# Optimization experiments

Hardware: AMD Instinct MI355X
Metric: run time of the kernel (lower is better)

Reference implementation:

```python
import jax, jax.numpy as jnp
import numpy as np

D_MODEL = 512
N_HEADS = 8
D_HEAD = D_MODEL // N_HEADS
SCALE = D_HEAD ** -0.5


def _rel_shift(x):
    # x: (b, h, qlen, klen) -> Transformer-XL relative shift
    b, h, qlen, klen = x.shape
    x = jnp.pad(x, ((0, 0), (0, 0), (0, 0), (1, 0)))        # (b,h,q,k+1)
    x = x.reshape(b, h, klen + 1, qlen)
    x = x[:, :, 1:, :].reshape(b, h, qlen, klen)
    return x


def setup_inputs() -> dict:
    key = jax.random.key(0)
    ks = jax.random.split(key, 12)
    B, S = 2, 2048
    P = 2 * S - 1
    w = lambda k, shape: (jax.random.normal(k, shape, jnp.float32) * 0.02)
    return {
        "x": jax.random.normal(ks[0], (B, S, D_MODEL), jnp.float32),
        "pos_emb": jax.random.normal(ks[1], (P, D_MODEL), jnp.float32),
        "Wq": w(ks[2], (D_MODEL, D_MODEL)), "bq": jnp.zeros((D_MODEL,), jnp.float32),
        "Wk": w(ks[3], (D_MODEL, D_MODEL)), "bk": jnp.zeros((D_MODEL,), jnp.float32),
        "Wv": w(ks[4], (D_MODEL, D_MODEL)), "bv": jnp.zeros((D_MODEL,), jnp.float32),
        "Wp": w(ks[5], (D_MODEL, D_MODEL)),
        "Wo": w(ks[6], (D_MODEL, D_MODEL)), "bo": jnp.zeros((D_MODEL,), jnp.float32),
        "pos_bias_u": w(ks[7], (N_HEADS, D_HEAD)),
        "pos_bias_v": w(ks[8], (N_HEADS, D_HEAD)),
    }


def reference(x, pos_emb, Wq, bq, Wk, bk, Wv, bv, Wp, Wo, bo, pos_bias_u, pos_bias_v):
    B, S, _ = x.shape
    # projections (torch Linear: y = x @ W^T + b; here W stored as (in, out))
    q = (x @ Wq + bq).reshape(B, S, N_HEADS, D_HEAD)
    k = (x @ Wk + bk).reshape(B, S, N_HEADS, D_HEAD)
    v = (x @ Wv + bv).reshape(B, S, N_HEADS, D_HEAD)
    p = (pos_emb @ Wp).reshape(-1, N_HEADS, D_HEAD)  # (2S-1, H, D)

    # content score: (q + u) @ k^T  -> (B,H,S,S)
    content = jnp.einsum("bshd,bthd->bhst", q + pos_bias_u, k)
    # position score: (q + v_bias) @ p^T -> (B,H,S,2S-1), then rel_shift
    pos = jnp.einsum("bshd,phd->bhsp", q + pos_bias_v, p)
    pos = _rel_shift(pos)[..., :S]  # trim to kv_len

    attn = jax.nn.softmax((content + pos) * SCALE, axis=-1)
    out = jnp.einsum("bhst,bthd->bshd", attn, v).reshape(B, S, D_MODEL)
    out = out @ Wo + bo
    return out
```

## Files before the change

### kernel.cpp

```cpp
#include <hip/hip_runtime.h>

#define DM    512
#define NH    8
#define DH    64
#define SEQ   2048
#define PLEN  4095
#define NB    2
#define ATT_SCALE 0.125f

typedef __attribute__((ext_vector_type(8))) _Float16 half8;
typedef __attribute__((ext_vector_type(4))) float   floatx4;

__device__ __forceinline__ void gll16(const _Float16* g, _Float16* l) {
    __builtin_amdgcn_global_load_lds(
        (const __attribute__((address_space(1))) void*)g,
        (__attribute__((address_space(3))) void*)l, 16, 0, 0);
}

__global__ __launch_bounds__(256)
void prep(const float* __restrict__ x, const float* __restrict__ pe,
          const float* __restrict__ W0, const float* __restrict__ W1,
          const float* __restrict__ W2, const float* __restrict__ W3,
          const float* __restrict__ W4,
          _Float16* __restrict__ x16, _Float16* __restrict__ pe16,
          _Float16* __restrict__ Wt)
{
    __shared__ _Float16 tile[64 * 72];
    const int z = blockIdx.z;
    const int t = threadIdx.x;

    if (z < 2) {
        const float* src = z ? pe : x;
        _Float16* dst = z ? pe16 : x16;
        const long n = z ? (long)PLEN * DM : (long)NB * SEQ * DM;
        const long i = ((long)blockIdx.x * 256 + t) * 8;
        if (i >= n) return;
        float4 f0 = *(const float4*)(src + i);
        float4 f1 = *(const float4*)(src + i + 4);
        half8 o;
        o[0] = (_Float16)f0.x; o[1] = (_Float16)f0.y;
        o[2] = (_Float16)f0.z; o[3] = (_Float16)f0.w;
        o[4] = (_Float16)f1.x; o[5] = (_Float16)f1.y;
        o[6] = (_Float16)f1.z; o[7] = (_Float16)f1.w;
        *(half8*)(dst + i) = o;
        return;
    }
    if (blockIdx.x >= 64) return;
    const int wz = z - 2;
    const float* W = (wz == 0) ? W0 : (wz == 1) ? W1 : (wz == 2) ? W2
                   : (wz == 3) ? W3 : W4;
    _Float16* dst_base = Wt + (size_t)wz * DM * DM;
    const int n0 = (blockIdx.x & 7) * 64, k0 = (blockIdx.x >> 3) * 64;
    {
        const int kr = t >> 2, nch = (t & 3) * 16;
        const float* src = W + (size_t)(k0 + kr) * DM + n0 + nch;
        float4 f0 = *(const float4*)(src + 0);
        float4 f1 = *(const float4*)(src + 4);
        float4 f2 = *(const float4*)(src + 8);
        float4 f3 = *(const float4*)(src + 12);
        _Float16* trow = &tile[kr * 72 + nch];
        trow[0]  = (_Float16)f0.x; trow[1]  = (_Float16)f0.y;
        trow[2]  = (_Float16)f0.z; trow[3]  = (_Float16)f0.w;
        trow[4]  = (_Float16)f1.x; trow[5]  = (_Float16)f1.y;
        trow[6]  = (_Float16)f1.z; trow[7]  = (_Float16)f1.w;
        trow[8]  = (_Float16)f2.x; trow[9]  = (_Float16)f2.y;
        trow[10] = (_Float16)f2.z; trow[11] = (_Float16)f2.w;
        trow[12] = (_Float16)f3.x; trow[13] = (_Float16)f3.y;
        trow[14] = (_Float16)f3.z; trow[15] = (_Float16)f3.w;
    }
    __syncthreads();
    {
        const int nr = t >> 2, kch = (t & 3) * 16;
        half8 o0, o1;
#pragma unroll
        for (int i = 0; i < 8; ++i) o0[i] = tile[(kch + i) * 72 + nr];
#pragma unroll
        for (int i = 0; i < 8; ++i) o1[i] = tile[(kch + 8 + i) * 72 + nr];
        _Float16* dst = dst_base + (size_t)(n0 + nr) * DM + k0 + kch;
        *(half8*)dst = o0;
        *(half8*)(dst + 8) = o1;
    }
}

__global__ __launch_bounds__(256)
void gemm_qkvp(const _Float16* __restrict__ X, const _Float16* __restrict__ Pe,
               const _Float16* __restrict__ Wt,
               const float* __restrict__ bq, const float* __restrict__ bk,
               const float* __restrict__ bv, const float* __restrict__ bu,
               const float* __restrict__ bvb,
               _Float16* __restrict__ qu16, _Float16* __restrict__ qv16,
               _Float16* __restrict__ k16, _Float16* __restrict__ vt16,
               _Float16* __restrict__ p16)
{
    __shared__ _Float16 smem[32768];

    const int t = threadIdx.x;
    const int w = t >> 6, lane = t & 63, quad = lane >> 4, l16 = lane & 15;
    const int wr = w >> 1, wc = w & 1;
    const int l3 = lane >> 3, pos = lane & 7;
    const int z = blockIdx.z;
    const int n0 = blockIdx.x * 128;
    const int m0 = blockIdx.y * 128;

    const _Float16* A = (z == 3) ? Pe : X;
    const _Float16* Wz = Wt + (size_t)z * DM * DM;

    const int kx = l16 & 7;
    const int hox0 = ((quad) ^ kx) * 8;
    const int hox1 = ((4 + quad) ^ kx) * 8;

    floatx4 acc[4][4];
#pragma unroll
    for (int i = 0; i < 4; ++i)
#pragma unroll
        for (int j = 0; j < 4; ++j) acc[i][j] = (floatx4){0.f, 0.f, 0.f, 0.f};

#define QSTAGE(CUR, K0)                                                        \
    { _Float16* aB = smem + (CUR) * 16384;                                     \
      _Float16* wB = aB + 8192;                                                \
      _Pragma("unroll") for (int I = 0; I < 4; ++I) {                          \
        const int gr = I * 32 + w * 8 + l3;                                    \
        const int ch = pos ^ l3;                                               \
        int ar = m0 + gr; if (z == 3 && ar > PLEN - 1) ar = PLEN - 1;          \
        gll16(A + (size_t)ar * DM + (K0) + ch * 8, aB + I * 2048 + w * 512);   \
        gll16(Wz + (size_t)(n0 + gr) * DM + (K0) + ch * 8,                     \
              wB + I * 2048 + w * 512); } }

    QSTAGE(0, 0);
    int cur = 0;
    for (int k0 = 0; k0 < DM; k0 += 64) {
        asm volatile("s_waitcnt vmcnt(0)" ::: "memory");
        __builtin_amdgcn_s_barrier();
        asm volatile("" ::: "memory");
        if (k0 + 64 < DM) QSTAGE(cur ^ 1, k0 + 64);
        const _Float16* aB = smem + cur * 16384;
        const _Float16* wB = aB + 8192;
#pragma unroll
        for (int kb = 0; kb < 2; ++kb) {
            const int hox = kb ? hox1 : hox0;
            half8 af[4], bf[4];
#pragma unroll
            for (int i = 0; i < 4; ++i)
                af[i] = *(const half8*)&aB[(wr * 64 + i * 16 + l16) * 64 + hox];
#pragma unroll
            for (int j = 0; j < 4; ++j)
                bf[j] = *(const half8*)&wB[(wc * 64 + j * 16 + l16) * 64 + hox];
#pragma unroll
            for (int i = 0; i < 4; ++i)
#pragma unroll
                for (int j = 0; j < 4; ++j)
                    acc[i][j] = __builtin_amdgcn_mfma_f32_16x16x32_f16(
                        af[i], bf[j], acc[i][j], 0, 0, 0);
        }
        cur ^= 1;
    }
#undef QSTAGE

    const int hh = (n0 >> 6) + wc;
    const int bb = m0 >> 11;
    const int sbase = (m0 & 2047) + wr * 64;

    if (z == 0) {
#pragma unroll
        for (int j = 0; j < 4; ++j) {
            const int n = n0 + wc * 64 + j * 16 + l16;
            const float bval = bq[n], uval = bu[n], vval = bvb[n];
#pragma unroll
            for (int i = 0; i < 4; ++i)
#pragma unroll
                for (int r = 0; r < 4; ++r) {
                    const int s = sbase + i * 16 + 4 * quad + r;
                    const size_t dst = ((size_t)((hh * NB + bb) * SEQ) + s) * DH + (n & 63);
                    const float q = acc[i][j][r] + bval;
                    qu16[dst] = (_Float16)((q + uval) * ATT_SCALE);
                    qv16[dst] = (_Float16)((q + vval) * ATT_SCALE);
                }
        }
    } else if (z == 1) {
#pragma unroll
        for (int j = 0; j < 4; ++j) {
            const int n = n0 + wc * 64 + j * 16 + l16;
            const float bval = bk[n];
#pragma unroll
            for (int i = 0; i < 4; ++i)
#pragma unroll
                for (int r = 0; r < 4; ++r) {
                    const int s = sbase + i * 16 + 4 * quad + r;
                    k16[((size_t)((hh * NB + bb) * SEQ) + s) * DH + (n & 63)] =
                        (_Float16)(acc[i][j][r] + bval);
                }
        }
    } else if (z == 2) {
        __syncthreads();
        _Float16* tr = smem;
#pragma unroll
        for (int j = 0; j < 4; ++j) {
            const int ncol = wc * 64 + j * 16 + l16;
            const float bval = bv[n0 + ncol];
#pragma unroll
            for (int i = 0; i < 4; ++i)
#pragma unroll
                for (int r = 0; r < 4; ++r)
                    tr[(wr * 64 + i * 16 + 4 * quad + r) * 132 + ncol] =
                        (_Float16)(acc[i][j][r] + bval);
        }
        __syncthreads();
        {
            const int col = t >> 1;
            const int half = t & 1;
            const int h2 = (n0 + col) >> 6, d = (n0 + col) & 63;
            const int s0 = (m0 & 2047) + half * 64;
            _Float16* dst = vt16 + ((size_t)((h2 * NB + bb) * DH) + d) * SEQ + s0;
#pragma unroll
            for (int c = 0; c < 8; ++c) {
                half8 o;
#pragma unroll
                for (int k = 0; k < 8; ++k)
                    o[k] = tr[(half * 64 + c * 8 + k) * 132 + col];
                *(half8*)(dst + c * 8) = o;
            }
        }
    } else {
#pragma unroll
        for (int j = 0; j < 4; ++j) {
            const int n = n0 + wc * 64 + j * 16 + l16;
#pragma unroll
            for (int i = 0; i < 4; ++i)
#pragma unroll
                for (int r = 0; r < 4; ++r) {
                    const int m = m0 + wr * 64 + i * 16 + 4 * quad + r;
                    if (m < PLEN)
                        p16[((size_t)hh * PLEN + m) * DH + (n & 63)] =
                            (_Float16)acc[i][j][r];
                }
        }
    }
}

__global__ __launch_bounds__(256, 3)
void relattn_mfma(const _Float16* __restrict__ QU,
                  const _Float16* __restrict__ QV,
                  const _Float16* __restrict__ Kp,
                  const _Float16* __restrict__ VT,
                  const _Float16* __restrict__ Pp,
                  float* __restrict__ Opart,
                  float* __restrict__ Lpart)
{
    __shared__ _Float16 kbuf[2 * 4096];
    __shared__ _Float16 vbuf[4096];
    __shared__ _Float16 pring[2 * 4096];
    __shared__ _Float16 tS[64 * 72];

    const int t = threadIdx.x;
    const int w = t >> 6, lane = t & 63, quad = lane >> 4, l16 = lane & 15;

    const int bid = blockIdx.x;
    const int swz = (bid & 7) * 128 + (bid >> 3);
    const int i0 = (swz & 31) * 64;
    const int h  = (swz >> 5) & 7;
    const int zz = swz >> 8;
    const int b = zz & 1, jh = zz >> 1;

    const size_t hb = (size_t)(h * NB + b);
    const int cbase = 48 - 16 * w;
    const int jbeg = jh * (SEQ / 2), jend = jbeg + (SEQ / 2);

    half8 qa[2], va[2];
    {
        const _Float16* qrow = QU + (hb * SEQ + i0 + 16 * w + l16) * DH + quad * 8;
        const _Float16* vrow = QV + (hb * SEQ + i0 + 16 * w + l16) * DH + quad * 8;
        qa[0] = *(const half8*)qrow;       qa[1] = *(const half8*)(qrow + 32);
        va[0] = *(const half8*)vrow;       va[1] = *(const half8*)(vrow + 32);
    }

    floatx4 O[4];
    float lsum[4] = {0.f, 0.f, 0.f, 0.f};
#pragma unroll
    for (int ct = 0; ct < 4; ++ct) O[ct] = (floatx4){0.f, 0.f, 0.f, 0.f};

    const _Float16* Kbase = Kp + hb * SEQ * DH;
    const _Float16* Vbase = VT + hb * DH * SEQ;
    const _Float16* Pbase = Pp + (size_t)h * PLEN * DH;
    const int rbase0 = (SEQ - 1) - i0 - 63;
    const int w0beg  = rbase0 + jbeg;

    const int kx = l16 & 7;
    const int hox0 = ((quad) ^ kx) * 8;
    const int hox1 = ((4 + quad) ^ kx) * 8;

    const int l3 = lane >> 3, pos = lane & 7;

    int prow64[5], pcar[5];
#pragma unroll
    for (int c2 = 0; c2 < 5; ++c2) {
        const int off = cbase + 16 * c2 + l16;
        prow64[c2] = (off & 63) * 64;
        pcar[c2]   = (off >> 6) & 1;
    }

#define STAGE_K(DST, J0)                                                       \
    { _Pragma("unroll") for (int I = 0; I < 2; ++I) {                          \
        const int cid = w * 2 + I;                                             \
        const int row = cid * 8 + l3;                                          \
        gll16(Kbase + (size_t)((J0) + row) * DH + ((pos ^ l3) << 3),           \
              (DST) + cid * 512); } }

#define STAGE_V(J0)                                                            \
    { _Pragma("unroll") for (int I = 0; I < 2; ++I) {                          \
        const int cid = w * 2 + I;                                             \
        const int row = cid * 8 + l3;                                          \
        gll16(Vbase + (size_t)row * SEQ + (J0) + ((pos ^ l3) << 3),            \
              vbuf + cid * 512); } }

#define STAGE_P(RELB)                                                         \
    { _Float16* pdst = pring + ((((RELB) >> 6) & 1) * 4096);                  \
      _Pragma("unroll") for (int I = 0; I < 2; ++I) {                         \
        const int cid = w * 2 + I;                                            \
        int ar = w0beg + (RELB) + cid * 8 + l3;                               \
        if (ar > PLEN - 1) ar = PLEN - 1;                                     \
        gll16(Pbase + (size_t)ar * DH + ((pos ^ l3) << 3),                    \
              pdst + cid * 512); } }

    STAGE_K(kbuf, jbeg);
    STAGE_P(0);
    STAGE_P(64);

    int cur = 0, par = 0;
    for (int j0 = jbeg; j0 < jend; j0 += 64) {
        asm volatile("s_waitcnt vmcnt(0)" ::: "memory");
        __builtin_amdgcn_s_barrier();
        asm volatile("" ::: "memory");

        const _Float16* kS = kbuf + cur * 4096;
        const bool more = (j0 + 64 < jend);

        STAGE_V(j0);
        if (more) STAGE_K(kbuf + (cur ^ 1) * 4096, j0 + 64);

        floatx4 Tacc[5];
#pragma unroll
        for (int c2 = 0; c2 < 5; ++c2) Tacc[c2] = (floatx4){0.f, 0.f, 0.f, 0.f};
#pragma unroll
        for (int c2 = 0; c2 < 5; ++c2) {
            const _Float16* pp = pring + ((pcar[c2] ^ par) * 4096) + prow64[c2];
            half8 bf0 = *(const half8*)(pp + hox0);
            half8 bf1 = *(const half8*)(pp + hox1);
            Tacc[c2] = __builtin_amdgcn_mfma_f32_16x16x32_f16(va[0], bf0, Tacc[c2], 0, 0, 0);
            Tacc[c2] = __builtin_amdgcn_mfma_f32_16x16x32_f16(va[1], bf1, Tacc[c2], 0, 0, 0);
        }

        floatx4 Sc[4];
#pragma unroll
        for (int ct = 0; ct < 4; ++ct) Sc[ct] = (floatx4){0.f, 0.f, 0.f, 0.f};
#pragma unroll
        for (int ct = 0; ct < 4; ++ct) {
            half8 bf0 = *(const half8*)&kS[(16 * ct + l16) * 64 + hox0];
            half8 bf1 = *(const half8*)&kS[(16 * ct + l16) * 64 + hox1];
            Sc[ct] = __builtin_amdgcn_mfma_f32_16x16x32_f16(qa[0], bf0, Sc[ct], 0, 0, 0);
            Sc[ct] = __builtin_amdgcn_mfma_f32_16x16x32_f16(qa[1], bf1, Sc[ct], 0, 0, 0);
        }

#pragma unroll
        for (int r = 0; r < 4; ++r) {
            const int u  = l16 - 4 * quad - r + 15;
            const int dl = u & 15;
            const int s  = u >> 4;
            const int pidx = (((quad << 4) | dl) << 2);
            float rot[5];
#pragma unroll
            for (int c2 = 0; c2 < 5; ++c2)
                rot[c2] = __int_as_float(__builtin_amdgcn_ds_bpermute(
                    pidx, __float_as_int(Tacc[c2][r])));
#pragma unroll
            for (int ct = 0; ct < 4; ++ct) {
                const float tv = s ? rot[ct + 1] : rot[ct];
                const float e = __expf(Sc[ct][r] + tv);
                Sc[ct][r] = e;
                lsum[r] += e;
            }
        }

#pragma unroll
        for (int ct = 0; ct < 4; ++ct)
#pragma unroll
            for (int r = 0; r < 4; ++r)
                tS[(16 * w + 4 * quad + r) * 72 + 16 * ct + l16] = (_Float16)Sc[ct][r];
        asm volatile("" ::: "memory");

        if (more) asm volatile("s_waitcnt vmcnt(2)" ::: "memory");
        else      asm volatile("s_waitcnt vmcnt(0)" ::: "memory");
        __builtin_amdgcn_s_barrier();
        asm volatile("" ::: "memory");

        if (more) STAGE_P((j0 - jbeg) + 128);

#pragma unroll
        for (int kb = 0; kb < 2; ++kb) {
            half8 af = *(const half8*)&tS[(16 * w + l16) * 72 + kb * 32 + quad * 8];
            const int hox = kb ? hox1 : hox0;
#pragma unroll
            for (int ct = 0; ct < 4; ++ct) {
                half8 bf = *(const half8*)&vbuf[(16 * ct + l16) * 64 + hox];
                O[ct] = __builtin_amdgcn_mfma_f32_16x16x32_f16(af, bf, O[ct], 0, 0, 0);
            }
        }
        asm volatile("" ::: "memory");
        cur ^= 1; par ^= 1;
    }
#undef STAGE_K
#undef STAGE_V
#undef STAGE_P

    float* Op = Opart + (size_t)jh * NB * SEQ * DM;
    float* Lp = Lpart + (size_t)jh * NH * NB * SEQ;
#pragma unroll
    for (int r = 0; r < 4; ++r) {
#pragma unroll
        for (int m = 1; m < 16; m <<= 1) lsum[r] += __shfl_xor(lsum[r], m);
        const int row = i0 + 16 * w + 4 * quad + r;
        if (l16 == 0) Lp[hb * SEQ + row] = lsum[r];
        float* orow = Op + (size_t)(b * SEQ + row) * DM + h * DH;
#pragma unroll
        for (int ct = 0; ct < 4; ++ct)
            orow[16 * ct + l16] = O[ct][r];
    }
}

__global__ __launch_bounds__(256)
void gemm_out(const float* __restrict__ O0, const float* __restrict__ O1,
              const float* __restrict__ L0, const float* __restrict__ L1,
              const _Float16* __restrict__ Wt,
              const float* __restrict__ bias, float* __restrict__ Out)
{
    __shared__ _Float16 aS[64 * 72];
    __shared__ _Float16 wS[64 * 72];

    const int t = threadIdx.x;
    const int w = t >> 6, lane = t & 63, quad = lane >> 4, l16 = lane & 15;

    const int bid = blockIdx.x;
    const int swzb = (bid & 7) * 64 + (bid >> 3);
    const int n0 = (swzb & 7) * 64;
    const int m0 = (swzb >> 3) * 64;
    const int srow = t >> 2, sch = (t & 3) * 16;

    const int mrow = m0 + srow;
    const int bA = mrow >> 11, sA = mrow & 2047;
    const float* o0p = O0 + (size_t)mrow * DM + sch;
    const float* o1p = O1 + (size_t)mrow * DM + sch;
    const _Float16* wrowp = Wt + (size_t)(n0 + srow) * DM + sch;

    floatx4 acc[4];
#pragma unroll
    for (int ct = 0; ct < 4; ++ct) acc[ct] = (floatx4){0.f, 0.f, 0.f, 0.f};

    float4 pa0 = *(const float4*)(o0p + 0);
    float4 pa1 = *(const float4*)(o0p + 4);
    float4 pa2 = *(const float4*)(o0p + 8);
    float4 pa3 = *(const float4*)(o0p + 12);
    float4 pc0 = *(const float4*)(o1p + 0);
    float4 pc1 = *(const float4*)(o1p + 4);
    float4 pc2 = *(const float4*)(o1p + 8);
    float4 pc3 = *(const float4*)(o1p + 12);
    half8 pw0 = *(const half8*)wrowp;
    half8 pw1 = *(const half8*)(wrowp + 8);

    for (int k0 = 0; k0 < DM; k0 += 64) {
        __syncthreads();
        const int hA = k0 >> 6;
        const int li = (hA * NB + bA) * SEQ + sA;
        const float inv = 1.f / (L0[li] + L1[li]);
        half8 h0, h1;
        h0[0] = (_Float16)((pa0.x + pc0.x) * inv);
        h0[1] = (_Float16)((pa0.y + pc0.y) * inv);
        h0[2] = (_Float16)((pa0.z + pc0.z) * inv);
        h0[3] = (_Float16)((pa0.w + pc0.w) * inv);
        h0[4] = (_Float16)((pa1.x + pc1.x) * inv);
        h0[5] = (_Float16)((pa1.y + pc1.y) * inv);
        h0[6] = (_Float16)((pa1.z + pc1.z) * inv);
        h0[7] = (_Float16)((pa1.w + pc1.w) * inv);
        h1[0] = (_Float16)((pa2.x + pc2.x) * inv);
        h1[1] = (_Float16)((pa2.y + pc2.y) * inv);
        h1[2] = (_Float16)((pa2.z + pc2.z) * inv);
        h1[3] = (_Float16)((pa2.w + pc2.w) * inv);
        h1[4] = (_Float16)((pa3.x + pc3.x) * inv);
        h1[5] = (_Float16)((pa3.y + pc3.y) * inv);
        h1[6] = (_Float16)((pa3.z + pc3.z) * inv);
        h1[7] = (_Float16)((pa3.w + pc3.w) * inv);
        *(half8*)&aS[srow * 72 + sch]     = h0;
        *(half8*)&aS[srow * 72 + sch + 8] = h1;
        *(half8*)&wS[srow * 72 + sch]     = pw0;
        *(half8*)&wS[srow * 72 + sch + 8] = pw1;
        __syncthreads();
        if (k0 + 64 < DM) {
            pa0 = *(const float4*)(o0p + k0 + 64);
            pa1 = *(const float4*)(o0p + k0 + 68);
            pa2 = *(const float4*)(o0p + k0 + 72);
            pa3 = *(const float4*)(o0p + k0 + 76);
            pc0 = *(const float4*)(o1p + k0 + 64);
            pc1 = *(const float4*)(o1p + k0 + 68);
            pc2 = *(const float4*)(o1p + k0 + 72);
            pc3 = *(const float4*)(o1p + k0 + 76);
            pw0 = *(const half8*)(wrowp + k0 + 64);
            pw1 = *(const half8*)(wrowp + k0 + 72);
        }
#pragma unroll
        for (int kb = 0; kb < 2; ++kb) {
            half8 af = *(const half8*)&aS[(16 * w + l16) * 72 + kb * 32 + quad * 8];
#pragma unroll
            for (int ct = 0; ct < 4; ++ct) {
                half8 bf = *(const half8*)&wS[(16 * ct + l16) * 72 + kb * 32 + quad * 8];
                acc[ct] = __builtin_amdgcn_mfma_f32_16x16x32_f16(af, bf, acc[ct], 0, 0, 0);
            }
        }
    }

#pragma unroll
    for (int ct = 0; ct < 4; ++ct) {
        const int n = n0 + 16 * ct + l16;
        const float bval = bias[n];
#pragma unroll
        for (int r = 0; r < 4; ++r) {
            const int m = m0 + 16 * w + 4 * quad + r;
            Out[(size_t)m * DM + n] = acc[ct][r] + bval;
        }
    }
}

extern "C" void kernel_launch(void* const* d_in, const int* in_sizes, int n_in,
                              void* d_out, int out_size, void* d_ws, size_t ws_size,
                              hipStream_t stream)
{
    (void)in_sizes; (void)n_in; (void)out_size; (void)ws_size;
    const float* x   = (const float*)d_in[0];
    const float* pe  = (const float*)d_in[1];
    const float* Wq  = (const float*)d_in[2];
    const float* bq  = (const float*)d_in[3];
    const float* Wk  = (const float*)d_in[4];
    const float* bk  = (const float*)d_in[5];
    const float* Wv  = (const float*)d_in[6];
    const float* bv  = (const float*)d_in[7];
    const float* Wp  = (const float*)d_in[8];
    const float* Wo  = (const float*)d_in[9];
    const float* bo  = (const float*)d_in[10];
    const float* pbu = (const float*)d_in[11];
    const float* pbv = (const float*)d_in[12];
    float* out = (float*)d_out;

    const size_t nX  = (size_t)NB * SEQ * DM;
    const size_t nPe = (size_t)PLEN * DM;
    const size_t nW  = (size_t)DM * DM;
    const size_t nH  = (size_t)NH * NB * SEQ * DH;
    const size_t nPh = (size_t)NH * PLEN * DH;
    const size_t nL  = (size_t)NH * NB * SEQ;

    _Float16* x16  = (_Float16*)d_ws;
    _Float16* pe16 = x16 + nX;
    _Float16* wt   = pe16 + nPe;
    _Float16* qu16 = wt + 5 * nW;
    _Float16* qv16 = qu16 + nH;
    _Float16* k16  = qv16 + nH;
    _Float16* vt16 = k16 + nH;
    _Float16* p16  = vt16 + nH;
    _Float16* ow16 = p16 + nPh;
    float*    opart = (float*)(ow16 + nX);
    float*    lpart = opart + 2 * nX;

    dim3 blk(256);
    prep<<<dim3(1024, 1, 7), blk, 0, stream>>>(x, pe, Wq, Wk, Wv, Wp, Wo,
                                               x16, pe16, wt);
    gemm_qkvp<<<dim3(4, 32, 4), blk, 0, stream>>>(x16, pe16, wt,
                                                  bq, bk, bv, pbu, pbv,
                                                  qu16, qv16, k16, vt16, p16);
    relattn_mfma<<<dim3(1024), blk, 0, stream>>>(
        qu16, qv16, k16, vt16, p16, opart, lpart);
    gemm_out<<<dim3(512), blk, 0, stream>>>(opart, opart + nX,
                                            lpart, lpart + nL,
                                            wt + 4 * nW, bo, out);
}
```

Measured before the change: 180.1 us.

## Process two 64-row query tiles per attention block to reuse K/V/P tiles

Each attention workgroup now covers 128 query rows (two 64-row sub-tiles) instead of 64, so each staged K, V and position tile in LDS serves twice as many rows. The position ring grows to three buffers because the two sub-tiles need overlapping windows of the relative-position table. V fragments are loaded into registers once and shared by both PV products. The grid is halved and the occupancy hint is dropped, which raises register and LDS pressure and may lower occupancy and latency hiding.

New measurement: 180.0 us. About the same (-0.0%).

```diff
diff --git a/kernel.cpp b/kernel.cpp
--- a/kernel.cpp
+++ b/kernel.cpp
@@ -237,7 +237,7 @@
     }
 }
 
-__global__ __launch_bounds__(256, 3)
+__global__ __launch_bounds__(256)
 void relattn_mfma(const _Float16* __restrict__ QU,
                   const _Float16* __restrict__ QV,
                   const _Float16* __restrict__ Kp,
@@ -248,41 +248,48 @@
 {
     __shared__ _Float16 kbuf[2 * 4096];
     __shared__ _Float16 vbuf[4096];
-    __shared__ _Float16 pring[2 * 4096];
+    __shared__ _Float16 pring[3 * 4096];
     __shared__ _Float16 tS[64 * 72];
 
     const int t = threadIdx.x;
     const int w = t >> 6, lane = t & 63, quad = lane >> 4, l16 = lane & 15;
 
     const int bid = blockIdx.x;
-    const int swz = (bid & 7) * 128 + (bid >> 3);
-    const int i0 = (swz & 31) * 64;
-    const int h  = (swz >> 5) & 7;
-    const int zz = swz >> 8;
+    const int swz = (bid & 7) * 64 + (bid >> 3);
+    const int i0 = (swz & 15) * 128;
+    const int h  = (swz >> 4) & 7;
+    const int zz = swz >> 7;
     const int b = zz & 1, jh = zz >> 1;
 
     const size_t hb = (size_t)(h * NB + b);
     const int cbase = 48 - 16 * w;
     const int jbeg = jh * (SEQ / 2), jend = jbeg + (SEQ / 2);
 
-    half8 qa[2], va[2];
+    half8 qa0[2], va0[2], qa1[2], va1[2];
     {
-        const _Float16* qrow = QU + (hb * SEQ + i0 + 16 * w + l16) * DH + quad * 8;
-        const _Float16* vrow = QV + (hb * SEQ + i0 + 16 * w + l16) * DH + quad * 8;
-        qa[0] = *(const half8*)qrow;       qa[1] = *(const half8*)(qrow + 32);
-        va[0] = *(const half8*)vrow;       va[1] = *(const half8*)(vrow + 32);
-    }
-
-    floatx4 O[4];
-    float lsum[4] = {0.f, 0.f, 0.f, 0.f};
-#pragma unroll
-    for (int ct = 0; ct < 4; ++ct) O[ct] = (floatx4){0.f, 0.f, 0.f, 0.f};
+        const _Float16* q0 = QU + (hb * SEQ + i0 + 16 * w + l16) * DH + quad * 8;
+        const _Float16* v0 = QV + (hb * SEQ + i0 + 16 * w + l16) * DH + quad * 8;
+        const _Float16* q1 = q0 + (size_t)64 * DH;
+        const _Float16* v1 = v0 + (size_t)64 * DH;
+        qa0[0] = *(const half8*)q0;  qa0[1] = *(const half8*)(q0 + 32);
+        va0[0] = *(const half8*)v0;  va0[1] = *(const half8*)(v0 + 32);
+        qa1[0] = *(const half8*)q1;  qa1[1] = *(const half8*)(q1 + 32);
+        va1[0] = *(const half8*)v1;  va1[1] = *(const half8*)(v1 + 32);
+    }
+
+    floatx4 O0[4], O1[4];
+    float lsum0[4] = {0.f, 0.f, 0.f, 0.f};
+    float lsum1[4] = {0.f, 0.f, 0.f, 0.f};
+#pragma unroll
+    for (int ct = 0; ct < 4; ++ct) {
+        O0[ct] = (floatx4){0.f, 0.f, 0.f, 0.f};
+        O1[ct] = (floatx4){0.f, 0.f, 0.f, 0.f};
+    }
 
     const _Float16* Kbase = Kp + hb * SEQ * DH;
     const _Float16* Vbase = VT + hb * DH * SEQ;
     const _Float16* Pbase = Pp + (size_t)h * PLEN * DH;
-    const int rbase0 = (SEQ - 1) - i0 - 63;
-    const int w0beg  = rbase0 + jbeg;
+    const int w0 = (SEQ - 1) - (i0 + 64) - 63 + jbeg;
 
     const int kx = l16 & 7;
     const int hox0 = ((quad) ^ kx) * 8;
@@ -312,20 +319,24 @@
         gll16(Vbase + (size_t)row * SEQ + (J0) + ((pos ^ l3) << 3),            \
               vbuf + cid * 512); } }
 
-#define STAGE_P(RELB)                                                         \
-    { _Float16* pdst = pring + ((((RELB) >> 6) & 1) * 4096);                  \
-      _Pragma("unroll") for (int I = 0; I < 2; ++I) {                         \
+#define STAGE_P_TO(PDST, RELB)                                                \
+    { _Pragma("unroll") for (int I = 0; I < 2; ++I) {                         \
         const int cid = w * 2 + I;                                            \
-        int ar = w0beg + (RELB) + cid * 8 + l3;                               \
+        int ar = w0 + (RELB) + cid * 8 + l3;                                  \
         if (ar > PLEN - 1) ar = PLEN - 1;                                     \
         gll16(Pbase + (size_t)ar * DH + ((pos ^ l3) << 3),                    \
-              pdst + cid * 512); } }
+              (PDST) + cid * 512); } }
+
+    _Float16* r0 = pring;
+    _Float16* r1 = pring + 4096;
+    _Float16* r2 = pring + 8192;
 
     STAGE_K(kbuf, jbeg);
-    STAGE_P(0);
-    STAGE_P(64);
-
-    int cur = 0, par = 0;
+    STAGE_P_TO(r0, 0);
+    STAGE_P_TO(r1, 64);
+    STAGE_P_TO(r2, 128);
+
+    int cur = 0;
     for (int j0 = jbeg; j0 < jend; j0 += 64) {
         asm volatile("s_waitcnt vmcnt(0)" ::: "memory");
         __builtin_amdgcn_s_barrier();
@@ -337,27 +348,43 @@
         STAGE_V(j0);
         if (more) STAGE_K(kbuf + (cur ^ 1) * 4096, j0 + 64);
 
-        floatx4 Tacc[5];
-#pragma unroll
-        for (int c2 = 0; c2 < 5; ++c2) Tacc[c2] = (floatx4){0.f, 0.f, 0.f, 0.f};
+        floatx4 Tacc0[5], Tacc1[5];
 #pragma unroll
         for (int c2 = 0; c2 < 5; ++c2) {
-            const _Float16* pp = pring + ((pcar[c2] ^ par) * 4096) + prow64[c2];
-            half8 bf0 = *(const half8*)(pp + hox0);
-            half8 bf1 = *(const half8*)(pp + hox1);
-            Tacc[c2] = __builtin_amdgcn_mfma_f32_16x16x32_f16(va[0], bf0, Tacc[c2], 0, 0, 0);
-            Tacc[c2] = __builtin_amdgcn_mfma_f32_16x16x32_f16(va[1], bf1, Tacc[c2], 0, 0, 0);
-        }
-
-        floatx4 Sc[4];
-#pragma unroll
-        for (int ct = 0; ct < 4; ++ct) Sc[ct] = (floatx4){0.f, 0.f, 0.f, 0.f};
+            Tacc0[c2] = (floatx4){0.f, 0.f, 0.f, 0.f};
+            Tacc1[c2] = (floatx4){0.f, 0.f, 0.f, 0.f};
+        }
+#pragma unroll
+        for (int c2 = 0; c2 < 5; ++c2) {
+            const _Float16* pp1 = (pcar[c2] ? r1 : r0) + prow64[c2];
+            half8 bf0 = *(const half8*)(pp1 + hox0);
+            half8 bf1 = *(const half8*)(pp1 + hox1);
+            Tacc1[c2] = __builtin_amdgcn_mfma_f32_16x16x32_f16(va1[0], bf0, Tacc1[c2], 0, 0, 0);
+            Tacc1[c2] = __builtin_amdgcn_mfma_f32_16x16x32_f16(va1[1], bf1, Tacc1[c2], 0, 0, 0);
+        }
+#pragma unroll
+        for (int c2 = 0; c2 < 5; ++c2) {
+            const _Float16* pp0 = (pcar[c2] ? r2 : r1) + prow64[c2];
+            half8 bf0 = *(const half8*)(pp0 + hox0);
+            half8 bf1 = *(const half8*)(pp0 + hox1);
+            Tacc0[c2] = __builtin_amdgcn_mfma_f32_16x16x32_f16(va0[0], bf0, Tacc0[c2], 0, 0, 0);
+            Tacc0[c2] = __builtin_amdgcn_mfma_f32_16x16x32_f16(va0[1], bf1, Tacc0[c2], 0, 0, 0);
+        }
+
+        floatx4 Sc0[4], Sc1[4];
+#pragma unroll
+        for (int ct = 0; ct < 4; ++ct) {
+            Sc0[ct] = (floatx4){0.f, 0.f, 0.f, 0.f};
+            Sc1[ct] = (floatx4){0.f, 0.f, 0.f, 0.f};
+        }
 #pragma unroll
         for (int ct = 0; ct < 4; ++ct) {
             half8 bf0 = *(const half8*)&kS[(16 * ct + l16) * 64 + hox0];
             half8 bf1 = *(const half8*)&kS[(16 * ct + l16) * 64 + hox1];
-            Sc[ct] = __builtin_amdgcn_mfma_f32_16x16x32_f16(qa[0], bf0, Sc[ct], 0, 0, 0);
-            Sc[ct] = __builtin_amdgcn_mfma_f32_16x16x32_f16(qa[1], bf1, Sc[ct], 0, 0, 0);
+            Sc0[ct] = __builtin_amdgcn_mfma_f32_16x16x32_f16(qa0[0], bf0, Sc0[ct], 0, 0, 0);
+            Sc0[ct] = __builtin_amdgcn_mfma_f32_16x16x32_f16(qa0[1], bf1, Sc0[ct], 0, 0, 0);
+            Sc1[ct] = __builtin_amdgcn_mfma_f32_16x16x32_f16(qa1[0], bf0, Sc1[ct], 0, 0, 0);
+            Sc1[ct] = __builtin_amdgcn_mfma_f32_16x16x32_f16(qa1[1], bf1, Sc1[ct], 0, 0, 0);
         }
 
 #pragma unroll
@@ -370,59 +397,109 @@
 #pragma unroll
             for (int c2 = 0; c2 < 5; ++c2)
                 rot[c2] = __int_as_float(__builtin_amdgcn_ds_bpermute(
-                    pidx, __float_as_int(Tacc[c2][r])));
+                    pidx, __float_as_int(Tacc0[c2][r])));
 #pragma unroll
             for (int ct = 0; ct < 4; ++ct) {
                 const float tv = s ? rot[ct + 1] : rot[ct];
-                const float e = __expf(Sc[ct][r] + tv);
-                Sc[ct][r] = e;
-                lsum[r] += e;
+                const float e = __expf(Sc0[ct][r] + tv);
+                Sc0[ct][r] = e;
+                lsum0[r] += e;
             }
         }
-
 #pragma unroll
         for (int ct = 0; ct < 4; ++ct)
 #pragma unroll
             for (int r = 0; r < 4; ++r)
-                tS[(16 * w + 4 * quad + r) * 72 + 16 * ct + l16] = (_Float16)Sc[ct][r];
+                tS[(16 * w + 4 * quad + r) * 72 + 16 * ct + l16] = (_Float16)Sc0[ct][r];
         asm volatile("" ::: "memory");
+
+#pragma unroll
+        for (int r = 0; r < 4; ++r) {
+            const int u  = l16 - 4 * quad - r + 15;
+            const int dl = u & 15;
+            const int s  = u >> 4;
+            const int pidx = (((quad << 4) | dl) << 2);
+            float rot[5];
+#pragma unroll
+            for (int c2 = 0; c2 < 5; ++c2)
+                rot[c2] = __int_as_float(__builtin_amdgcn_ds_bpermute(
+                    pidx, __float_as_int(Tacc1[c2][r])));
+#pragma unroll
+            for (int ct = 0; ct < 4; ++ct) {
+                const float tv = s ? rot[ct + 1] : rot[ct];
+                const float e = __expf(Sc1[ct][r] + tv);
+                Sc1[ct][r] = e;
+                lsum1[r] += e;
+            }
+        }
 
         if (more) asm volatile("s_waitcnt vmcnt(2)" ::: "memory");
         else      asm volatile("s_waitcnt vmcnt(0)" ::: "memory");
         __builtin_amdgcn_s_barrier();
         asm volatile("" ::: "memory");
 
-        if (more) STAGE_P((j0 - jbeg) + 128);
-
+        if (more) STAGE_P_TO(r0, (j0 - jbeg) + 192);
+
+        half8 vf0[4], vf1[4];
+#pragma unroll
+        for (int ct = 0; ct < 4; ++ct) {
+            vf0[ct] = *(const half8*)&vbuf[(16 * ct + l16) * 64 + hox0];
+            vf1[ct] = *(const half8*)&vbuf[(16 * ct + l16) * 64 + hox1];
+        }
 #pragma unroll
         for (int kb = 0; kb < 2; ++kb) {
             half8 af = *(const half8*)&tS[(16 * w + l16) * 72 + kb * 32 + quad * 8];
-            const int hox = kb ? hox1 : hox0;
-#pragma unroll
-            for (int ct = 0; ct < 4; ++ct) {
-                half8 bf = *(const half8*)&vbuf[(16 * ct + l16) * 64 + hox];
-                O[ct] = __builtin_amdgcn_mfma_f32_16x16x32_f16(af, bf, O[ct], 0, 0, 0);
-            }
-        }
+#pragma unroll
+            for (int ct = 0; ct < 4; ++ct)
+                O0[ct] = __builtin_amdgcn_mfma_f32_16x16x32_f16(
+                    af, kb ? vf1[ct] : vf0[ct], O0[ct], 0, 0, 0);
+        }
+#pragma unroll
+        for (int ct = 0; ct < 4; ++ct)
+#pragma unroll
+            for (int r = 0; r < 4; ++r)
+                tS[(16 * w + 4 * quad + r) * 72 + 16 * ct + l16] = (_Float16)Sc1[ct][r];
         asm volatile("" ::: "memory");
-        cur ^= 1; par ^= 1;
+#pragma unroll
+        for (int kb = 0; kb < 2; ++kb) {
+            half8 af = *(const half8*)&tS[(16 * w + l16) * 72 + kb * 32 + quad * 8];
+#pragma unroll
+            for (int ct = 0; ct < 4; ++ct)
+                O1[ct] = __builtin_amdgcn_mfma_f32_16x16x32_f16(
+                    af, kb ? vf1[ct] : vf0[ct], O1[ct], 0, 0, 0);
+        }
+        asm volatile("" ::: "memory");
+
+        { _Float16* tmp = r0; r0 = r1; r1 = r2; r2 = tmp; }
+        cur ^= 1;
     }
 #undef STAGE_K
 #undef STAGE_V
-#undef STAGE_P
+#undef STAGE_P_TO
 
     float* Op = Opart + (size_t)jh * NB * SEQ * DM;
     float* Lp = Lpart + (size_t)jh * NH * NB * SEQ;
 #pragma unroll
     for (int r = 0; r < 4; ++r) {
 #pragma unroll
-        for (int m = 1; m < 16; m <<= 1) lsum[r] += __shfl_xor(lsum[r], m);
+        for (int m = 1; m < 16; m <<= 1) lsum0[r] += __shfl_xor(lsum0[r], m);
         const int row = i0 + 16 * w + 4 * quad + r;
-        if (l16 == 0) Lp[hb * SEQ + row] = lsum[r];
+        if (l16 == 0) Lp[hb * SEQ + row] = lsum0[r];
         float* orow = Op + (size_t)(b * SEQ + row) * DM + h * DH;
 #pragma unroll
         for (int ct = 0; ct < 4; ++ct)
-            orow[16 * ct + l16] = O[ct][r];
+            orow[16 * ct + l16] = O0[ct][r];
+    }
+#pragma unroll
+    for (int r = 0; r < 4; ++r) {
+#pragma unroll
+        for (int m = 1; m < 16; m <<= 1) lsum1[r] += __shfl_xor(lsum1[r], m);
+        const int row = i0 + 64 + 16 * w + 4 * quad + r;
+        if (l16 == 0) Lp[hb * SEQ + row] = lsum1[r];
+        float* orow = Op + (size_t)(b * SEQ + row) * DM + h * DH;
+#pragma unroll
+        for (int ct = 0; ct < 4; ++ct)
+            orow[16 * ct + l16] = O1[ct][r];
     }
 }
 
@@ -572,7 +649,7 @@
     gemm_qkvp<<<dim3(4, 32, 4), blk, 0, stream>>>(x16, pe16, wt,
                                                   bq, bk, bv, pbu, pbv,
                                                   qu16, qv16, k16, vt16, p16);
-    relattn_mfma<<<dim3(1024), blk, 0, stream>>>(
+    relattn_mfma<<<dim3(512), blk, 0, stream>>>(
         qu16, qv16, k16, vt16, p16, opart, lpart);
     gemm_out<<<dim3(512), blk, 0, stream>>>(opart, opart + nX,
                                             lpart, lpart + nL,
```

## Software-pipeline score MFMAs across iterations with a triple-buffered position ring

Applied to the files above, without the earlier changes.

Restructures the attention loop so the position-score and content-score MFMAs for the next tile are issued inside the current iteration, overlapping them with the softmax and PV work. The position ring grows from two to three LDS buffers, rotated by pointer swap, and the P prefetch now runs one tile further ahead. The launch-bounds occupancy hint of 3 blocks per CU is dropped because more LDS and registers are needed. The cost is lower occupancy and longer live ranges for Tacc and Sc, and the loop now waits for all outstanding loads (vmcnt(0)) at the mid-loop barrier instead of vmcnt(2).

Result: slower. 206.9 us (+14.9%).

```diff
diff --git a/kernel.cpp b/kernel.cpp
--- a/kernel.cpp
+++ b/kernel.cpp
@@ -237,7 +237,7 @@
     }
 }
 
-__global__ __launch_bounds__(256, 3)
+__global__ __launch_bounds__(256)
 void relattn_mfma(const _Float16* __restrict__ QU,
                   const _Float16* __restrict__ QV,
                   const _Float16* __restrict__ Kp,
@@ -248,7 +248,7 @@
 {
     __shared__ _Float16 kbuf[2 * 4096];
     __shared__ _Float16 vbuf[4096];
-    __shared__ _Float16 pring[2 * 4096];
+    __shared__ _Float16 pring[3 * 4096];
     __shared__ _Float16 tS[64 * 72];
 
     const int t = threadIdx.x;
@@ -281,8 +281,7 @@
     const _Float16* Kbase = Kp + hb * SEQ * DH;
     const _Float16* Vbase = VT + hb * DH * SEQ;
     const _Float16* Pbase = Pp + (size_t)h * PLEN * DH;
-    const int rbase0 = (SEQ - 1) - i0 - 63;
-    const int w0beg  = rbase0 + jbeg;
+    const int w0 = (SEQ - 1) - i0 - 63 + jbeg;
 
     const int kx = l16 & 7;
     const int hox0 = ((quad) ^ kx) * 8;
@@ -312,53 +311,61 @@
         gll16(Vbase + (size_t)row * SEQ + (J0) + ((pos ^ l3) << 3),            \
               vbuf + cid * 512); } }
 
-#define STAGE_P(RELB)                                                         \
-    { _Float16* pdst = pring + ((((RELB) >> 6) & 1) * 4096);                  \
-      _Pragma("unroll") for (int I = 0; I < 2; ++I) {                         \
+#define STAGE_P_TO(PDST, RELB)                                                \
+    { _Pragma("unroll") for (int I = 0; I < 2; ++I) {                         \
         const int cid = w * 2 + I;                                            \
-        int ar = w0beg + (RELB) + cid * 8 + l3;                               \
+        int ar = w0 + (RELB) + cid * 8 + l3;                                  \
         if (ar > PLEN - 1) ar = PLEN - 1;                                     \
         gll16(Pbase + (size_t)ar * DH + ((pos ^ l3) << 3),                    \
-              pdst + cid * 512); } }
+              (PDST) + cid * 512); } }
+
+#define PHASE_A(TACC, LO, HI)                                                 \
+    { _Pragma("unroll")                                                       \
+      for (int c2 = 0; c2 < 5; ++c2) {                                        \
+        (TACC)[c2] = (floatx4){0.f, 0.f, 0.f, 0.f};                           \
+        const _Float16* pp = (pcar[c2] ? (HI) : (LO)) + prow64[c2];           \
+        half8 bf0 = *(const half8*)(pp + hox0);                               \
+        half8 bf1 = *(const half8*)(pp + hox1);                               \
+        (TACC)[c2] = __builtin_amdgcn_mfma_f32_16x16x32_f16(va[0], bf0, (TACC)[c2], 0, 0, 0); \
+        (TACC)[c2] = __builtin_amdgcn_mfma_f32_16x16x32_f16(va[1], bf1, (TACC)[c2], 0, 0, 0); } }
+
+#define PHASE_B(SC, KS)                                                       \
+    { _Pragma("unroll")                                                       \
+      for (int ct = 0; ct < 4; ++ct) {                                        \
+        (SC)[ct] = (floatx4){0.f, 0.f, 0.f, 0.f};                             \
+        half8 bf0 = *(const half8*)&(KS)[(16 * ct + l16) * 64 + hox0];        \
+        half8 bf1 = *(const half8*)&(KS)[(16 * ct + l16) * 64 + hox1];        \
+        (SC)[ct] = __builtin_amdgcn_mfma_f32_16x16x32_f16(qa[0], bf0, (SC)[ct], 0, 0, 0); \
+        (SC)[ct] = __builtin_amdgcn_mfma_f32_16x16x32_f16(qa[1], bf1, (SC)[ct], 0, 0, 0); } }
+
+    _Float16* pw0 = pring;
+    _Float16* pw1 = pring + 4096;
+    _Float16* pw2 = pring + 8192;
+
+    floatx4 Tacc[5], Sc[4];
 
     STAGE_K(kbuf, jbeg);
-    STAGE_P(0);
-    STAGE_P(64);
-
-    int cur = 0, par = 0;
-    for (int j0 = jbeg; j0 < jend; j0 += 64) {
+    STAGE_P_TO(pw0, 0);
+    STAGE_P_TO(pw1, 64);
+    STAGE_P_TO(pw2, 128);
+    asm volatile("s_waitcnt vmcnt(0)" ::: "memory");
+    __builtin_amdgcn_s_barrier();
+    asm volatile("" ::: "memory");
+    PHASE_A(Tacc, pw0, pw1);
+    PHASE_B(Sc, kbuf);
+
+    int cur = 0;
+    int tt = 0;
+    for (int j0 = jbeg; j0 < jend; j0 += 64, ++tt) {
+        const bool more = (j0 + 64 < jend);
+        _Float16* knext = kbuf + (cur ^ 1) * 4096;
+
         asm volatile("s_waitcnt vmcnt(0)" ::: "memory");
         __builtin_amdgcn_s_barrier();
         asm volatile("" ::: "memory");
 
-        const _Float16* kS = kbuf + cur * 4096;
-        const bool more = (j0 + 64 < jend);
-
         STAGE_V(j0);
-        if (more) STAGE_K(kbuf + (cur ^ 1) * 4096, j0 + 64);
-
-        floatx4 Tacc[5];
-#pragma unroll
-        for (int c2 = 0; c2 < 5; ++c2) Tacc[c2] = (floatx4){0.f, 0.f, 0.f, 0.f};
-#pragma unroll
-        for (int c2 = 0; c2 < 5; ++c2) {
-            const _Float16* pp = pring + ((pcar[c2] ^ par) * 4096) + prow64[c2];
-            half8 bf0 = *(const half8*)(pp + hox0);
-            half8 bf1 = *(const half8*)(pp + hox1);
-            Tacc[c2] = __builtin_amdgcn_mfma_f32_16x16x32_f16(va[0], bf0, Tacc[c2], 0, 0, 0);
-            Tacc[c2] = __builtin_amdgcn_mfma_f32_16x16x32_f16(va[1], bf1, Tacc[c2], 0, 0, 0);
-        }
-
-        floatx4 Sc[4];
-#pragma unroll
-        for (int ct = 0; ct < 4; ++ct) Sc[ct] = (floatx4){0.f, 0.f, 0.f, 0.f};
-#pragma unroll
-        for (int ct = 0; ct < 4; ++ct) {
-            half8 bf0 = *(const half8*)&kS[(16 * ct + l16) * 64 + hox0];
-            half8 bf1 = *(const half8*)&kS[(16 * ct + l16) * 64 + hox1];
-            Sc[ct] = __builtin_amdgcn_mfma_f32_16x16x32_f16(qa[0], bf0, Sc[ct], 0, 0, 0);
-            Sc[ct] = __builtin_amdgcn_mfma_f32_16x16x32_f16(qa[1], bf1, Sc[ct], 0, 0, 0);
-        }
+        if (more) STAGE_K(knext, j0 + 64);
 
 #pragma unroll
         for (int r = 0; r < 4; ++r) {
@@ -387,12 +394,13 @@
                 tS[(16 * w + 4 * quad + r) * 72 + 16 * ct + l16] = (_Float16)Sc[ct][r];
         asm volatile("" ::: "memory");
 
-        if (more) asm volatile("s_waitcnt vmcnt(2)" ::: "memory");
-        else      asm volatile("s_waitcnt vmcnt(0)" ::: "memory");
+        if (more) PHASE_A(Tacc, pw1, pw2);
+
+        asm volatile("s_waitcnt vmcnt(0)" ::: "memory");
         __builtin_amdgcn_s_barrier();
         asm volatile("" ::: "memory");
 
-        if (more) STAGE_P((j0 - jbeg) + 128);
+        if (more) STAGE_P_TO(pw0, 64 * (tt + 3));
 
 #pragma unroll
         for (int kb = 0; kb < 2; ++kb) {
@@ -405,11 +413,17 @@
             }
         }
         asm volatile("" ::: "memory");
-        cur ^= 1; par ^= 1;
+
+        if (more) PHASE_B(Sc, knext);
+
+        { _Float16* tmp = pw0; pw0 = pw1; pw1 = pw2; pw2 = tmp; }
+        cur ^= 1;
     }
 #undef STAGE_K
 #undef STAGE_V
-#undef STAGE_P
+#undef STAGE_P_TO
+#undef PHASE_A
+#undef PHASE_B
 
     float* Op = Opart + (size_t)jh * NB * SEQ * DM;
     float* Lp = Lpart + (size_t)jh * NH * NB * SEQ;
```
